# Kernel optimization log

Measured on AMD Instinct MI355X. Metric: run time of the kernel, lower is better.

Reference implementation:

```python
import jax, jax.numpy as jnp
import numpy as np

EPS = 1e-8
LN_EPS = 1e-6
B, S_IN, F, D, NH, MLP, L, O = 32, 512, 16, 512, 8, 2048, 4, 8
HD = D // NH

def softplus(x):
    return jnp.log1p(jnp.exp(x))

def apply_rope(x):
    # x: [B, S, D]; RoPE over full d_model, as in the original
    S, d = x.shape[1], x.shape[2]
    x1, x2 = x[..., ::2], x[..., 1::2]
    theta = jnp.arange(S)[:, None] / 10000 ** (jnp.arange(0, d, 2) / d)
    c, s = jnp.cos(theta)[None], jnp.sin(theta)[None]
    x1r = x1 * c - x2 * s
    x2r = x1 * s + x2 * c
    return jnp.stack([x1r, x2r], axis=-1).reshape(x.shape)

def layer_norm(x, g, b):
    mu = jnp.mean(x, axis=-1, keepdims=True)
    var = jnp.mean(jnp.square(x - mu), axis=-1, keepdims=True)
    return (x - mu) * jax.lax.rsqrt(var + LN_EPS) * g + b

def setup_inputs() -> dict:
    key = jax.random.key(0)
    ks = jax.random.split(key, 32)
    n = jax.random.normal
    d = {
        "x": n(ks[0], (B, S_IN, F), jnp.float32),
        "W_in": n(ks[1], (F, D)) * (1.0 / np.sqrt(F)),
        "b_in": jnp.zeros((D,)),
        "cls_tokens": n(ks[2], (1, O, D)) * 0.02,
        "Wqkv": n(ks[3], (L, D, 3 * D)) * (1.0 / np.sqrt(D)),
        "bqkv": jnp.zeros((L, 3 * D)),
        "Wo": n(ks[4], (L, D, D)) * (1.0 / np.sqrt(D)),
        "bo": jnp.zeros((L, D)),
        "ln1_g": jnp.ones((L, D)), "ln1_b": jnp.zeros((L, D)),
        "Wm1": n(ks[5], (L, D, MLP)) * (1.0 / np.sqrt(D)),
        "bm1": jnp.zeros((L, MLP)),
        "Wm2": n(ks[6], (L, MLP, D)) * (1.0 / np.sqrt(MLP)),
        "bm2": jnp.zeros((L, D)),
        "ln2_g": jnp.ones((L, D)), "ln2_b": jnp.zeros((L, D)),
        "Wh": n(ks[7], (O, D, D)) * (1.0 / np.sqrt(D)),
        "bh": jnp.zeros((O, D)),
        "mu_wmu": n(ks[8], (O, D)) * (1.0 / np.sqrt(D)),
        "mu_wrho": n(ks[9], (O, D)) * 0.001,
        "mu_bmu": jnp.zeros((O,)),
        "mu_brho": n(ks[10], (O,)) * 0.001,
        "lv_wmu": n(ks[11], (O, D)) * (1.0 / np.sqrt(D)),
        "lv_wrho": n(ks[12], (O, D)) * 0.001,
        "lv_bmu": jnp.zeros((O,)),
        "lv_brho": n(ks[13], (O,)) * 0.001,
        "eps_mu_w": n(ks[14], (O, D)),
        "eps_mu_b": n(ks[15], (O,)),
        "eps_lv_w": n(ks[16], (O, D)),
        "eps_lv_b": n(ks[17], (O,)),
    }
    return d

def reference(x, W_in, b_in, cls_tokens, Wqkv, bqkv, Wo, bo, ln1_g, ln1_b,
              Wm1, bm1, Wm2, bm2, ln2_g, ln2_b, Wh, bh,
              mu_wmu, mu_wrho, mu_bmu, mu_brho,
              lv_wmu, lv_wrho, lv_bmu, lv_brho,
              eps_mu_w, eps_mu_b, eps_lv_w, eps_lv_b):
    h = x @ W_in + b_in                                     # [B, S_IN, D]
    cls = jnp.tile(cls_tokens, (h.shape[0], 1, 1))
    h = jnp.concatenate([cls, h], axis=1)                   # [B, S, D]
    Bt, S, d = h.shape
    for l in range(L):
        qkv = h @ Wqkv[l] + bqkv[l]
        q, k, v = jnp.split(qkv, 3, axis=-1)
        q, k = apply_rope(q), apply_rope(k)
        q = q.reshape(Bt, S, NH, HD).transpose(0, 2, 1, 3)
        k = k.reshape(Bt, S, NH, HD).transpose(0, 2, 1, 3)
        v = v.reshape(Bt, S, NH, HD).transpose(0, 2, 1, 3)
        scores = jnp.einsum('bhid,bhjd->bhij', q, k) / jnp.sqrt(jnp.float32(HD))
        attn = jax.nn.softmax(scores, axis=-1)              # dropout off (eval)
        out = jnp.einsum('bhij,bhjd->bhid', attn, v)
        out = out.transpose(0, 2, 1, 3).reshape(Bt, S, d)
        out = out @ Wo[l] + bo[l]
        h = layer_norm(h + out, ln1_g[l], ln1_b[l])
        m = jax.nn.relu(h @ Wm1[l] + bm1[l]) @ Wm2[l] + bm2[l]
        h = layer_norm(h + m, ln2_g[l], ln2_b[l])
    x_cls = h[:, :O, :]                                     # [B, O, D]
    hid = jax.nn.relu(jnp.einsum('bod,odh->boh', x_cls, Wh) + bh[None])
    def var_head(wmu, wrho, bmu, brho, ew, eb):
        w = wmu + (softplus(wrho) + EPS) * ew               # [O, D]
        b = bmu + (softplus(brho) + EPS) * eb               # [O]
        return jnp.einsum('boh,oh->bo', hid, w) + b[None]
    mu = var_head(mu_wmu, mu_wrho, mu_bmu, mu_brho, eps_mu_w, eps_mu_b)
    lv = var_head(lv_wmu, lv_wrho, lv_bmu, lv_brho, eps_lv_w, eps_lv_b)
    lv = jnp.log(EPS + softplus(lv))
    return (mu, lv)
```

## Files before the change

kernel.cpp:

```cpp
#include <hip/hip_runtime.h>
#include <cstdint>


#define BATCH   32
#define SEQ     520
#define SP      576
#define DIM     512
#define NHEAD   8
#define HDIM    64
#define MLPD    2048
#define NLAYER  4
#define NROW    (BATCH * SEQ)
#define NPAIR   256

typedef __attribute__((ext_vector_type(4))) float  f32x4;
typedef __attribute__((ext_vector_type(8))) short  short8;

__device__ __forceinline__ unsigned short f2bf(float f) {
    unsigned u = __float_as_uint(f);
    unsigned r = (u + 0x7fffu + ((u >> 16) & 1u)) >> 16;
    return (unsigned short)r;
}
__device__ __forceinline__ float bf2f(short s) {
    return __uint_as_float(((unsigned)(unsigned short)s) << 16);
}
__device__ __forceinline__ float wred_sum(float v) {
    #pragma unroll
    for (int off = 32; off; off >>= 1) v += __shfl_xor(v, off);
    return v;
}

__device__ __forceinline__ void gload16(const void* g, void* l) {
    __builtin_amdgcn_global_load_lds(
        (const __attribute__((address_space(1))) unsigned int*)g,
        (__attribute__((address_space(3))) unsigned int*)l,
        16, 0, 0);
}

__global__ __launch_bounds__(256) void k_wconv(const float* __restrict__ src,
                                               short* __restrict__ dst,
                                               int K, int N) {
    src += (size_t)blockIdx.z * K * N;
    dst += (size_t)blockIdx.z * K * N;
    int n0 = blockIdx.x * 64, k0 = blockIdx.y * 64;
    __shared__ float t[64][65];
    int tid = threadIdx.x;
    int r = tid >> 2, cq = (tid & 3) * 16;
    const float* sp = src + (size_t)(k0 + r) * N + n0 + cq;
    #pragma unroll
    for (int e = 0; e < 16; e += 4) {
        float4 v = *(const float4*)(sp + e);
        t[r][cq + e] = v.x; t[r][cq + e + 1] = v.y;
        t[r][cq + e + 2] = v.z; t[r][cq + e + 3] = v.w;
    }
    __syncthreads();
    int n = tid >> 2, kq = (tid & 3) * 16;
    short* dp = dst + (size_t)(n0 + n) * K + k0 + kq;
    short8 o0, o1;
    #pragma unroll
    for (int e = 0; e < 8; e++) o0[e] = (short)f2bf(t[kq + e][n]);
    #pragma unroll
    for (int e = 0; e < 8; e++) o1[e] = (short)f2bf(t[kq + 8 + e][n]);
    *(short8*)dp = o0;
    *(short8*)(dp + 8) = o1;
}

__global__ void k_rope_tab(float2* __restrict__ tab) {
    int s = blockIdx.x, i = threadIdx.x;
    float fr = powf(10000.f, -2.f * (float)i / 512.f);
    float th = (float)s * fr;
    float sn, cn;
    sincosf(th, &sn, &cn);
    tab[s * NPAIR + i] = make_float2(cn, sn);
}

__global__ __launch_bounds__(256) void k_in_proj(const float* __restrict__ x,
                                                 const float* __restrict__ Wi,
                                                 const float* __restrict__ bi,
                                                 const float* __restrict__ cls,
                                                 short* __restrict__ hb) {
    int row = blockIdx.x;
    int b = row / SEQ, s = row % SEQ;
    bool is_cls = s < 8;
    float xr[16];
    if (!is_cls) {
        const float* xp = x + (size_t)(b * 512 + (s - 8)) * 16;
        #pragma unroll
        for (int f = 0; f < 16; f++) xr[f] = xp[f];
    }
    for (int c = threadIdx.x; c < DIM; c += 256) {
        float v;
        if (is_cls) {
            v = cls[s * DIM + c];
        } else {
            v = bi[c];
            #pragma unroll
            for (int f = 0; f < 16; f++) v = fmaf(xr[f], Wi[f * DIM + c], v);
        }
        hb[(size_t)row * DIM + c] = (short)f2bf(v);
    }
}

template <int BK, bool RELU>
__global__ __launch_bounds__(256) void k_gemm(const short* __restrict__ A,
                                              const short* __restrict__ Bt,
                                              const float* __restrict__ bias,
                                              short* __restrict__ Cout,
                                              int N, int K) {
    constexpr int NB  = BK / 8;
    constexpr int MSK = NB - 1;
    constexpr int RPG = 1024 / (BK * 2);
    constexpr int GPW = 32 / RPG;
    __shared__ __align__(16) short As[2][128 * BK];
    __shared__ __align__(16) short Bs[2][128 * BK];
    const int tid = threadIdx.x;
    const int w = tid >> 6, l = tid & 63;

    const int chunk = gridDim.x >> 3;
    const int t = (blockIdx.x & 7) * chunk + (blockIdx.x >> 3);
    const int C = N >> 7;
    const int brow = (t / C) * 128, bcol = (t % C) * 128;

    const int srow = l / NB;
    const int sblk = l & MSK;
    const int soff = ((sblk ^ (srow & MSK)) * 8);
    const int fr = l & 15, t4 = l >> 4;
    const int wr = (w >> 1) * 64, wc = (w & 1) * 64;

    const short* Ab = A  + (size_t)(brow + w * 32 + srow) * K + soff;
    const short* Bb = Bt + (size_t)(bcol + w * 32 + srow) * K + soff;

    f32x4 acc[4][4];
    #pragma unroll
    for (int m = 0; m < 4; m++)
        #pragma unroll
        for (int n = 0; n < 4; n++) acc[m][n] = (f32x4){0.f, 0.f, 0.f, 0.f};

    auto stage = [&](int ko, int pb) {
        #pragma unroll
        for (int i = 0; i < GPW; i++)
            gload16(Ab + (size_t)(i * RPG) * K + ko,
                    &As[pb][(w * 32 + i * RPG) * BK]);
        #pragma unroll
        for (int i = 0; i < GPW; i++)
            gload16(Bb + (size_t)(i * RPG) * K + ko,
                    &Bs[pb][(w * 32 + i * RPG) * BK]);
    };

    const int nk = K / BK;
    stage(0, 0);
    __syncthreads();

    for (int kt = 0; kt < nk; ++kt) {
        const int cur = kt & 1;
        if (kt + 1 < nk) stage((kt + 1) * BK, cur ^ 1);
        __builtin_amdgcn_sched_barrier(0);

        short8 af[4][BK / 32], bf[4][BK / 32];
        #pragma unroll
        for (int m = 0; m < 4; m++) {
            int r = wr + m * 16 + fr;
            #pragma unroll
            for (int kk = 0; kk < BK / 32; kk++)
                af[m][kk] = *(const short8*)
                    &As[cur][r * BK + (((kk * 4 + t4) ^ (r & MSK)) * 8)];
        }
        #pragma unroll
        for (int n = 0; n < 4; n++) {
            int r = wc + n * 16 + fr;
            #pragma unroll
            for (int kk = 0; kk < BK / 32; kk++)
                bf[n][kk] = *(const short8*)
                    &Bs[cur][r * BK + (((kk * 4 + t4) ^ (r & MSK)) * 8)];
        }
        #pragma unroll
        for (int kk = 0; kk < BK / 32; kk++)
            #pragma unroll
            for (int m = 0; m < 4; m++)
                #pragma unroll
                for (int n = 0; n < 4; n++)
                    acc[m][n] = __builtin_amdgcn_mfma_f32_16x16x32_bf16(
                        af[m][kk], bf[n][kk], acc[m][n], 0, 0, 0);
        __syncthreads();
    }

    const int r0 = (l >> 4) * 4, c0 = l & 15;
    #pragma unroll
    for (int m = 0; m < 4; m++) {
        #pragma unroll
        for (int n = 0; n < 4; n++) {
            int col = bcol + wc + n * 16 + c0;
            float bv = bias[col];
            #pragma unroll
            for (int q = 0; q < 4; q++) {
                int row = brow + wr + m * 16 + r0 + q;
                float v = acc[m][n][q] + bv;
                if (RELU) v = fmaxf(v, 0.f);
                Cout[(size_t)row * N + col] = (short)f2bf(v);
            }
        }
    }
}

__global__ __launch_bounds__(256) void k_kvprep(const short* __restrict__ qkv,
                                                const float2* __restrict__ tab,
                                                short* __restrict__ kbuf,
                                                short* __restrict__ vtbuf) {
    int bx = blockIdx.x;
    int jt = bx % 9, bh = bx / 9, b = bh >> 3, h = bh & 7;
    int tid = threadIdx.x;
    int row = tid >> 2, ch = tid & 3;
    int s = jt * 64 + row;
    bool valid = s < SEQ;
    size_t g = (size_t)(b * SEQ + (valid ? s : 0)) * 1536;

    short8 ok0 = (short8)0, ok1 = (short8)0;
    if (valid) {
        short8 k0 = *(const short8*)(qkv + g + 512 + h * 64 + ch * 16);
        short8 k1 = *(const short8*)(qkv + g + 512 + h * 64 + ch * 16 + 8);
        #pragma unroll
        for (int pp = 0; pp < 4; pp++) {
            float2 cs = tab[s * NPAIR + h * 32 + ch * 8 + pp];
            float x1 = bf2f(k0[2 * pp]), x2 = bf2f(k0[2 * pp + 1]);
            ok0[2 * pp]     = (short)f2bf(x1 * cs.x - x2 * cs.y);
            ok0[2 * pp + 1] = (short)f2bf(x1 * cs.y + x2 * cs.x);
            cs = tab[s * NPAIR + h * 32 + ch * 8 + 4 + pp];
            x1 = bf2f(k1[2 * pp]); x2 = bf2f(k1[2 * pp + 1]);
            ok1[2 * pp]     = (short)f2bf(x1 * cs.x - x2 * cs.y);
            ok1[2 * pp + 1] = (short)f2bf(x1 * cs.y + x2 * cs.x);
        }
    }
    short* kd = kbuf + ((size_t)bh * SP + jt * 64 + row) * 64 + ch * 16;
    *(short8*)kd = ok0;
    *(short8*)(kd + 8) = ok1;

    __shared__ short vt[64][72];
    short8 v0 = (short8)0, v1 = (short8)0;
    if (valid) {
        v0 = *(const short8*)(qkv + g + 1024 + h * 64 + ch * 16);
        v1 = *(const short8*)(qkv + g + 1024 + h * 64 + ch * 16 + 8);
    }
    *(short8*)&vt[row][ch * 16] = v0;
    *(short8*)&vt[row][ch * 16 + 8] = v1;
    __syncthreads();
    int d = row;
    short8 w0, w1;
    #pragma unroll
    for (int e = 0; e < 8; e++) w0[e] = vt[ch * 16 + e][d];
    #pragma unroll
    for (int e = 0; e < 8; e++) w1[e] = vt[ch * 16 + 8 + e][d];
    short* vd = vtbuf + ((size_t)bh * 64 + d) * SP + jt * 64 + ch * 16;
    *(short8*)vd = w0;
    *(short8*)(vd + 8) = w1;
}

__global__ __launch_bounds__(256) void k_attn_mfma(const short* __restrict__ qkv,
                                                   const short* __restrict__ kbuf,
                                                   const short* __restrict__ vtbuf,
                                                   const float2* __restrict__ tab,
                                                   short* __restrict__ aob) {
    __shared__ __align__(16) short Kl[2][64 * 64];
    __shared__ __align__(16) short Vl[2][64 * 64];
    __shared__ __align__(16) short sP[4][16][72];
    const int tid = threadIdx.x;
    const int w = tid >> 6, l = tid & 63;
    const int c = l & 15, t4 = l >> 4;
    int bx = blockIdx.x;
    int qt = bx >> 8, bh = bx & 255, b = bh >> 3, h = bh & 7;

    int q0 = qt * 64 + w * 16;
    int qrow = q0 + c;
    int qr = qrow < SEQ ? qrow : SEQ - 1;
    size_t gq = (size_t)(b * SEQ + qr) * 1536 + h * 64;
    short8 qf0 = *(const short8*)(qkv + gq + t4 * 8);
    short8 qf1 = *(const short8*)(qkv + gq + 32 + t4 * 8);
    {
        const float2* tq = tab + (size_t)qr * NPAIR + h * 32;
        #pragma unroll
        for (int pp = 0; pp < 4; pp++) {
            float2 cs = tq[t4 * 4 + pp];
            float x1 = bf2f(qf0[2 * pp]), x2 = bf2f(qf0[2 * pp + 1]);
            qf0[2 * pp]     = (short)f2bf((x1 * cs.x - x2 * cs.y) * 0.125f);
            qf0[2 * pp + 1] = (short)f2bf((x1 * cs.y + x2 * cs.x) * 0.125f);
            cs = tq[16 + t4 * 4 + pp];
            x1 = bf2f(qf1[2 * pp]); x2 = bf2f(qf1[2 * pp + 1]);
            qf1[2 * pp]     = (short)f2bf((x1 * cs.x - x2 * cs.y) * 0.125f);
            qf1[2 * pp + 1] = (short)f2bf((x1 * cs.y + x2 * cs.x) * 0.125f);
        }
    }

    f32x4 o0 = {0,0,0,0}, o1 = {0,0,0,0}, o2 = {0,0,0,0}, o3 = {0,0,0,0};
    float mrow[4] = {-1e30f, -1e30f, -1e30f, -1e30f};
    float lrow[4] = {0.f, 0.f, 0.f, 0.f};

    const short* kb = kbuf + (size_t)bh * SP * 64;
    const short* vb = vtbuf + (size_t)bh * 64 * SP;
    const int r1 = w * 16 + (l >> 3);
    const int r2 = r1 + 8;
    const int blk = l & 7;

    auto stage = [&](int jt, int pb) {
        gload16(kb + ((size_t)(jt * 64 + r1)) * 64 + ((blk ^ (r1 & 7)) * 8),
                &Kl[pb][(w * 16) * 64]);
        gload16(kb + ((size_t)(jt * 64 + r2)) * 64 + ((blk ^ (r2 & 7)) * 8),
                &Kl[pb][(w * 16 + 8) * 64]);
        gload16(vb + (size_t)r1 * SP + jt * 64 + ((blk ^ (r1 & 7)) * 8),
                &Vl[pb][(w * 16) * 64]);
        gload16(vb + (size_t)r2 * SP + jt * 64 + ((blk ^ (r2 & 7)) * 8),
                &Vl[pb][(w * 16 + 8) * 64]);
    };

    stage(0, 0);
    __syncthreads();

    for (int jt = 0; jt < 9; jt++) {
        const int cur = jt & 1;
        if (jt + 1 < 9) stage(jt + 1, cur ^ 1);
        __builtin_amdgcn_sched_barrier(0);

        f32x4 s0 = {0,0,0,0}, s1 = {0,0,0,0}, s2 = {0,0,0,0}, s3 = {0,0,0,0};
        {
            int kr0 = c, kr1 = 16 + c, kr2 = 32 + c, kr3 = 48 + c;
            short8 kf;
            kf = *(const short8*)&Kl[cur][kr0 * 64 + ((t4 ^ (kr0 & 7)) * 8)];
            s0 = __builtin_amdgcn_mfma_f32_16x16x32_bf16(qf0, kf, s0, 0, 0, 0);
            kf = *(const short8*)&Kl[cur][kr0 * 64 + (((4 + t4) ^ (kr0 & 7)) * 8)];
            s0 = __builtin_amdgcn_mfma_f32_16x16x32_bf16(qf1, kf, s0, 0, 0, 0);
            kf = *(const short8*)&Kl[cur][kr1 * 64 + ((t4 ^ (kr1 & 7)) * 8)];
            s1 = __builtin_amdgcn_mfma_f32_16x16x32_bf16(qf0, kf, s1, 0, 0, 0);
            kf = *(const short8*)&Kl[cur][kr1 * 64 + (((4 + t4) ^ (kr1 & 7)) * 8)];
            s1 = __builtin_amdgcn_mfma_f32_16x16x32_bf16(qf1, kf, s1, 0, 0, 0);
            kf = *(const short8*)&Kl[cur][kr2 * 64 + ((t4 ^ (kr2 & 7)) * 8)];
            s2 = __builtin_amdgcn_mfma_f32_16x16x32_bf16(qf0, kf, s2, 0, 0, 0);
            kf = *(const short8*)&Kl[cur][kr2 * 64 + (((4 + t4) ^ (kr2 & 7)) * 8)];
            s2 = __builtin_amdgcn_mfma_f32_16x16x32_bf16(qf1, kf, s2, 0, 0, 0);
            kf = *(const short8*)&Kl[cur][kr3 * 64 + ((t4 ^ (kr3 & 7)) * 8)];
            s3 = __builtin_amdgcn_mfma_f32_16x16x32_bf16(qf0, kf, s3, 0, 0, 0);
            kf = *(const short8*)&Kl[cur][kr3 * 64 + (((4 + t4) ^ (kr3 & 7)) * 8)];
            s3 = __builtin_amdgcn_mfma_f32_16x16x32_bf16(qf1, kf, s3, 0, 0, 0);
        }

        if (jt == 8) {
            #pragma unroll
            for (int r = 0; r < 4; r++) {
                if (c >= 8) s0[r] = -1e30f;
                s1[r] = -1e30f; s2[r] = -1e30f; s3[r] = -1e30f;
            }
        }

        #pragma unroll
        for (int r = 0; r < 4; r++) {
            float mx = fmaxf(fmaxf(s0[r], s1[r]), fmaxf(s2[r], s3[r]));
            mx = fmaxf(mx, __shfl_xor(mx, 1));
            mx = fmaxf(mx, __shfl_xor(mx, 2));
            mx = fmaxf(mx, __shfl_xor(mx, 4));
            mx = fmaxf(mx, __shfl_xor(mx, 8));
            if (mx > mrow[r]) {
                float sc = __expf(mrow[r] - mx);
                mrow[r] = mx;
                lrow[r] *= sc;
                o0[r] *= sc; o1[r] *= sc; o2[r] *= sc; o3[r] *= sc;
            }
            float p0 = __expf(s0[r] - mrow[r]), p1 = __expf(s1[r] - mrow[r]);
            float p2 = __expf(s2[r] - mrow[r]), p3 = __expf(s3[r] - mrow[r]);
            float rs = p0 + p1 + p2 + p3;
            rs += __shfl_xor(rs, 1);
            rs += __shfl_xor(rs, 2);
            rs += __shfl_xor(rs, 4);
            rs += __shfl_xor(rs, 8);
            lrow[r] += rs;
            int q = t4 * 4 + r;
            sP[w][q][c]      = (short)f2bf(p0);
            sP[w][q][16 + c] = (short)f2bf(p1);
            sP[w][q][32 + c] = (short)f2bf(p2);
            sP[w][q][48 + c] = (short)f2bf(p3);
        }

        {
            short8 pf0 = *(const short8*)&sP[w][c][t4 * 8];
            short8 pf1 = *(const short8*)&sP[w][c][32 + t4 * 8];
            int vr0 = c, vr1 = 16 + c, vr2 = 32 + c, vr3 = 48 + c;
            short8 vf;
            vf = *(const short8*)&Vl[cur][vr0 * 64 + ((t4 ^ (vr0 & 7)) * 8)];
            o0 = __builtin_amdgcn_mfma_f32_16x16x32_bf16(pf0, vf, o0, 0, 0, 0);
            vf = *(const short8*)&Vl[cur][vr0 * 64 + (((4 + t4) ^ (vr0 & 7)) * 8)];
            o0 = __builtin_amdgcn_mfma_f32_16x16x32_bf16(pf1, vf, o0, 0, 0, 0);
            vf = *(const short8*)&Vl[cur][vr1 * 64 + ((t4 ^ (vr1 & 7)) * 8)];
            o1 = __builtin_amdgcn_mfma_f32_16x16x32_bf16(pf0, vf, o1, 0, 0, 0);
            vf = *(const short8*)&Vl[cur][vr1 * 64 + (((4 + t4) ^ (vr1 & 7)) * 8)];
            o1 = __builtin_amdgcn_mfma_f32_16x16x32_bf16(pf1, vf, o1, 0, 0, 0);
            vf = *(const short8*)&Vl[cur][vr2 * 64 + ((t4 ^ (vr2 & 7)) * 8)];
            o2 = __builtin_amdgcn_mfma_f32_16x16x32_bf16(pf0, vf, o2, 0, 0, 0);
            vf = *(const short8*)&Vl[cur][vr2 * 64 + (((4 + t4) ^ (vr2 & 7)) * 8)];
            o2 = __builtin_amdgcn_mfma_f32_16x16x32_bf16(pf1, vf, o2, 0, 0, 0);
            vf = *(const short8*)&Vl[cur][vr3 * 64 + ((t4 ^ (vr3 & 7)) * 8)];
            o3 = __builtin_amdgcn_mfma_f32_16x16x32_bf16(pf0, vf, o3, 0, 0, 0);
            vf = *(const short8*)&Vl[cur][vr3 * 64 + (((4 + t4) ^ (vr3 & 7)) * 8)];
            o3 = __builtin_amdgcn_mfma_f32_16x16x32_bf16(pf1, vf, o3, 0, 0, 0);
        }
        __syncthreads();
    }

    #pragma unroll
    for (int r = 0; r < 4; r++) {
        int q = q0 + t4 * 4 + r;
        if (q < SEQ) {
            float inv = 1.f / lrow[r];
            short* ao = aob + ((size_t)(b * SEQ + q)) * DIM + h * 64 + c;
            ao[0]  = (short)f2bf(o0[r] * inv);
            ao[16] = (short)f2bf(o1[r] * inv);
            ao[32] = (short)f2bf(o2[r] * inv);
            ao[48] = (short)f2bf(o3[r] * inv);
        }
    }
}

__global__ __launch_bounds__(256) void k_ln(short* __restrict__ hb,
                                            const short* __restrict__ delta,
                                            const float* __restrict__ g,
                                            const float* __restrict__ bta) {
    int row = blockIdx.x * 4 + (threadIdx.x >> 6);
    int l = threadIdx.x & 63;
    size_t base = (size_t)row * DIM + l * 8;
    short8 hv = *(const short8*)&hb[base];
    short8 dv = *(const short8*)&delta[base];
    float a[8];
    float s1 = 0.f, s2 = 0.f;
    #pragma unroll
    for (int e = 0; e < 8; e++) {
        a[e] = bf2f(hv[e]) + bf2f(dv[e]);
        s1 += a[e];
        s2 += a[e] * a[e];
    }
    s1 = wred_sum(s1);
    s2 = wred_sum(s2);
    float mu = s1 * (1.f / 512.f);
    float rr = rsqrtf(s2 * (1.f / 512.f) - mu * mu + 1e-6f);
    float4 g0 = *(const float4*)&g[l * 8];
    float4 g1 = *(const float4*)&g[l * 8 + 4];
    float4 b0 = *(const float4*)&bta[l * 8];
    float4 b1 = *(const float4*)&bta[l * 8 + 4];
    short8 o;
    o[0] = (short)f2bf((a[0] - mu) * rr * g0.x + b0.x);
    o[1] = (short)f2bf((a[1] - mu) * rr * g0.y + b0.y);
    o[2] = (short)f2bf((a[2] - mu) * rr * g0.z + b0.z);
    o[3] = (short)f2bf((a[3] - mu) * rr * g0.w + b0.w);
    o[4] = (short)f2bf((a[4] - mu) * rr * g1.x + b1.x);
    o[5] = (short)f2bf((a[5] - mu) * rr * g1.y + b1.y);
    o[6] = (short)f2bf((a[6] - mu) * rr * g1.z + b1.z);
    o[7] = (short)f2bf((a[7] - mu) * rr * g1.w + b1.w);
    *(short8*)&hb[base] = o;
}

__global__ __launch_bounds__(256) void k_hid(const short* __restrict__ hb,
                                             const float* __restrict__ Wh,
                                             const float* __restrict__ bh,
                                             float* __restrict__ hid) {
    int j = blockIdx.x * 256 + threadIdx.x;
    int o = blockIdx.y, b = blockIdx.z;
    const short* xr = hb + ((size_t)(b * SEQ + o)) * DIM;
    const float* wcol = Wh + (size_t)o * DIM * DIM + j;
    float acc = bh[o * DIM + j];
    #pragma unroll 8
    for (int d = 0; d < DIM; d++)
        acc = fmaf(bf2f(xr[d]), wcol[(size_t)d * DIM], acc);
    hid[((size_t)b * 8 + o) * DIM + j] = fmaxf(acc, 0.f);
}

__device__ __forceinline__ float softplus_f(float x) { return log1pf(expf(x)); }

__global__ __launch_bounds__(64) void k_var(const float* __restrict__ hid,
                                            const float* __restrict__ mu_wmu,
                                            const float* __restrict__ mu_wrho,
                                            const float* __restrict__ mu_bmu,
                                            const float* __restrict__ mu_brho,
                                            const float* __restrict__ lv_wmu,
                                            const float* __restrict__ lv_wrho,
                                            const float* __restrict__ lv_bmu,
                                            const float* __restrict__ lv_brho,
                                            const float* __restrict__ eps_mu_w,
                                            const float* __restrict__ eps_mu_b,
                                            const float* __restrict__ eps_lv_w,
                                            const float* __restrict__ eps_lv_b,
                                            float* __restrict__ out) {
    const float EPS = 1e-8f;
    int bo = blockIdx.x;
    int o = bo & 7;
    int l = threadIdx.x;
    float am = 0.f, al = 0.f;
    #pragma unroll
    for (int k = 0; k < 8; k++) {
        int d = k * 64 + l;
        int od = o * DIM + d;
        float hv = hid[(size_t)bo * DIM + d];
        am = fmaf(hv, mu_wmu[od] + (softplus_f(mu_wrho[od]) + EPS) * eps_mu_w[od], am);
        al = fmaf(hv, lv_wmu[od] + (softplus_f(lv_wrho[od]) + EPS) * eps_lv_w[od], al);
    }
    am = wred_sum(am);
    al = wred_sum(al);
    if (l == 0) {
        float mu = am + mu_bmu[o] + (softplus_f(mu_brho[o]) + EPS) * eps_mu_b[o];
        out[bo] = mu;
        float lvv = al + lv_bmu[o] + (softplus_f(lv_brho[o]) + EPS) * eps_lv_b[o];
        out[256 + bo] = logf(EPS + softplus_f(lvv));
    }
}

extern "C" void kernel_launch(void* const* d_in, const int* in_sizes, int n_in,
                              void* d_out, int out_size, void* d_ws, size_t ws_size,
                              hipStream_t stream) {
    const float* x      = (const float*)d_in[0];
    const float* W_in   = (const float*)d_in[1];
    const float* b_in   = (const float*)d_in[2];
    const float* cls    = (const float*)d_in[3];
    const float* Wqkv   = (const float*)d_in[4];
    const float* bqkv   = (const float*)d_in[5];
    const float* Wo     = (const float*)d_in[6];
    const float* bo     = (const float*)d_in[7];
    const float* ln1_g  = (const float*)d_in[8];
    const float* ln1_b  = (const float*)d_in[9];
    const float* Wm1    = (const float*)d_in[10];
    const float* bm1    = (const float*)d_in[11];
    const float* Wm2    = (const float*)d_in[12];
    const float* bm2    = (const float*)d_in[13];
    const float* ln2_g  = (const float*)d_in[14];
    const float* ln2_b  = (const float*)d_in[15];
    const float* Wh     = (const float*)d_in[16];
    const float* bh     = (const float*)d_in[17];
    const float* mu_wmu = (const float*)d_in[18];
    const float* mu_wrho= (const float*)d_in[19];
    const float* mu_bmu = (const float*)d_in[20];
    const float* mu_brho= (const float*)d_in[21];
    const float* lv_wmu = (const float*)d_in[22];
    const float* lv_wrho= (const float*)d_in[23];
    const float* lv_bmu = (const float*)d_in[24];
    const float* lv_brho= (const float*)d_in[25];
    const float* e_mu_w = (const float*)d_in[26];
    const float* e_mu_b = (const float*)d_in[27];
    const float* e_lv_w = (const float*)d_in[28];
    const float* e_lv_b = (const float*)d_in[29];
    float* out = (float*)d_out;

    char* p = (char*)d_ws;
    auto alloc = [&](size_t bytes) {
        char* r = p;
        p += (bytes + 255) & ~(size_t)255;
        return r;
    };
    const size_t qkv_bytes = (size_t)NROW * 1536 * 2;
    const size_t kbuf_bytes = (size_t)BATCH * NHEAD * SP * 64 * 2;
    const size_t attn_bytes = qkv_bytes + 2 * kbuf_bytes + 512;
    const size_t mid_bytes = (size_t)NROW * MLPD * 2;
    char*   U1    =          alloc(attn_bytes > mid_bytes ? attn_bytes : mid_bytes);
    short*  qkv   = (short*)U1;
    short*  kbuf  = (short*)(U1 + ((qkv_bytes + 255) & ~(size_t)255));
    short*  vtbuf = kbuf + kbuf_bytes / 2;
    short*  mid   = (short*)U1;
    short*  hb    = (short*) alloc((size_t)NROW * DIM * 2);
    short*  deltab= (short*) alloc((size_t)NROW * DIM * 2);
    short*  aob   = (short*) alloc((size_t)NROW * DIM * 2);
    short*  wqkvt = (short*) alloc((size_t)NLAYER * 1536 * 512 * 2);
    short*  wot   = (short*) alloc((size_t)NLAYER * 512 * 512 * 2);
    short*  wm1t  = (short*) alloc((size_t)NLAYER * 2048 * 512 * 2);
    short*  wm2t  = (short*) alloc((size_t)NLAYER * 512 * 2048 * 2);
    float2* ropet = (float2*)alloc((size_t)SEQ * NPAIR * 8);
    float*  hid   = (float*) alloc((size_t)256 * DIM * 4);

    k_wconv<<<dim3(24, 8, 4), 256, 0, stream>>>(Wqkv, wqkvt, 512, 1536);
    k_wconv<<<dim3(8, 8, 4),  256, 0, stream>>>(Wo,   wot,   512, 512);
    k_wconv<<<dim3(32, 8, 4), 256, 0, stream>>>(Wm1,  wm1t,  512, 2048);
    k_wconv<<<dim3(8, 32, 4), 256, 0, stream>>>(Wm2,  wm2t,  2048, 512);
    k_rope_tab<<<SEQ, NPAIR, 0, stream>>>(ropet);
    k_in_proj<<<NROW, 256, 0, stream>>>(x, W_in, b_in, cls, hb);

    const int RT = NROW / 128;
    for (int l = 0; l < NLAYER; l++) {
        k_gemm<32, false><<<RT * 12, 256, 0, stream>>>(
            hb, wqkvt + (size_t)l * 1536 * 512, bqkv + l * 1536, qkv, 1536, 512);
        k_kvprep<<<BATCH * NHEAD * 9, 256, 0, stream>>>(qkv, ropet, kbuf, vtbuf);
        k_attn_mfma<<<9 * 256, 256, 0, stream>>>(qkv, kbuf, vtbuf, ropet, aob);
        k_gemm<64, false><<<RT * 4, 256, 0, stream>>>(
            aob, wot + (size_t)l * 512 * 512, bo + l * 512, deltab, 512, 512);
        k_ln<<<NROW / 4, 256, 0, stream>>>(hb, deltab, ln1_g + l * 512, ln1_b + l * 512);
        k_gemm<32, true><<<RT * 16, 256, 0, stream>>>(
            hb, wm1t + (size_t)l * 2048 * 512, bm1 + l * 2048, mid, 2048, 512);
        k_gemm<64, false><<<RT * 4, 256, 0, stream>>>(
            mid, wm2t + (size_t)l * 512 * 2048, bm2 + l * 512, deltab, 512, 2048);
        k_ln<<<NROW / 4, 256, 0, stream>>>(hb, deltab, ln2_g + l * 512, ln2_b + l * 512);
    }

    k_hid<<<dim3(2, 8, 32), 256, 0, stream>>>(hb, Wh, bh, hid);
    k_var<<<256, 64, 0, stream>>>(hid, mu_wmu, mu_wrho, mu_bmu, mu_brho,
                                  lv_wmu, lv_wrho, lv_bmu, lv_brho,
                                  e_mu_w, e_mu_b, e_lv_w, e_lv_b, out);
}
```

Measured before the change: 1.232 ms.

## Fuse residual add into GEMM epilogue, use packed bf16 cvt and exp2 softmax

Moves the residual add from the layernorm kernels into the output-projection and MLP2 GEMM epilogues, so layernorm reads only one input tensor. Replaces software bf16 rounding with the hardware v_cvt_pk_bf16_f32 instruction across several kernels. Attention folds log2(e) into the Q scale, uses the hardware exp2, skips the row-max rescale when no lane exceeds the running max by more than a threshold, defers the row-sum shuffle reduction to the end, and raises wave priority around the MFMA blocks. The GEMM epilogue now does an extra strided read of the residual, and the lazy rescale lets exponents grow up to 2^8 before renormalising.

```diff
diff --git a/kernel.cpp b/kernel.cpp
--- a/kernel.cpp
+++ b/kernel.cpp
@@ -24,6 +24,16 @@
 __device__ __forceinline__ float bf2f(short s) {
     return __uint_as_float(((unsigned)(unsigned short)s) << 16);
 }
+__device__ __forceinline__ unsigned cvt_pk_bf16(float lo, float hi) {
+    unsigned r;
+    asm("v_cvt_pk_bf16_f32 %0, %1, %2" : "=v"(r) : "v"(lo), "v"(hi));
+    return r;
+}
+__device__ __forceinline__ float exp2_hw(float x) {
+    float r;
+    asm("v_exp_f32 %0, %1" : "=v"(r) : "v"(x));
+    return r;
+}
 __device__ __forceinline__ float wred_sum(float v) {
     #pragma unroll
     for (int off = 32; off; off >>= 1) v += __shfl_xor(v, off);
@@ -56,13 +66,15 @@
     __syncthreads();
     int n = tid >> 2, kq = (tid & 3) * 16;
     short* dp = dst + (size_t)(n0 + n) * K + k0 + kq;
-    short8 o0, o1;
-    #pragma unroll
-    for (int e = 0; e < 8; e++) o0[e] = (short)f2bf(t[kq + e][n]);
-    #pragma unroll
-    for (int e = 0; e < 8; e++) o1[e] = (short)f2bf(t[kq + 8 + e][n]);
-    *(short8*)dp = o0;
-    *(short8*)(dp + 8) = o1;
+    unsigned o0[4], o1[4];
+    #pragma unroll
+    for (int e = 0; e < 4; e++)
+        o0[e] = cvt_pk_bf16(t[kq + 2 * e][n], t[kq + 2 * e + 1][n]);
+    #pragma unroll
+    for (int e = 0; e < 4; e++)
+        o1[e] = cvt_pk_bf16(t[kq + 8 + 2 * e][n], t[kq + 9 + 2 * e][n]);
+    *(uint4*)dp = make_uint4(o0[0], o0[1], o0[2], o0[3]);
+    *(uint4*)(dp + 8) = make_uint4(o1[0], o1[1], o1[2], o1[3]);
 }
 
 __global__ void k_rope_tab(float2* __restrict__ tab) {
@@ -101,10 +113,11 @@
     }
 }
 
-template <int BK, bool RELU>
+template <int BK, bool RELU, bool ADDRES>
 __global__ __launch_bounds__(256) void k_gemm(const short* __restrict__ A,
                                               const short* __restrict__ Bt,
                                               const float* __restrict__ bias,
+                                              const short* __restrict__ Res,
                                               short* __restrict__ Cout,
                                               int N, int K) {
     constexpr int NB  = BK / 8;
@@ -195,6 +208,7 @@
             for (int q = 0; q < 4; q++) {
                 int row = brow + wr + m * 16 + r0 + q;
                 float v = acc[m][n][q] + bv;
+                if (ADDRES) v += bf2f(Res[(size_t)row * N + col]);
                 if (RELU) v = fmaxf(v, 0.f);
                 Cout[(size_t)row * N + col] = (short)f2bf(v);
             }
@@ -218,16 +232,16 @@
     if (valid) {
         short8 k0 = *(const short8*)(qkv + g + 512 + h * 64 + ch * 16);
         short8 k1 = *(const short8*)(qkv + g + 512 + h * 64 + ch * 16 + 8);
+        unsigned* u0 = (unsigned*)&ok0;
+        unsigned* u1 = (unsigned*)&ok1;
         #pragma unroll
         for (int pp = 0; pp < 4; pp++) {
             float2 cs = tab[s * NPAIR + h * 32 + ch * 8 + pp];
             float x1 = bf2f(k0[2 * pp]), x2 = bf2f(k0[2 * pp + 1]);
-            ok0[2 * pp]     = (short)f2bf(x1 * cs.x - x2 * cs.y);
-            ok0[2 * pp + 1] = (short)f2bf(x1 * cs.y + x2 * cs.x);
+            u0[pp] = cvt_pk_bf16(x1 * cs.x - x2 * cs.y, x1 * cs.y + x2 * cs.x);
             cs = tab[s * NPAIR + h * 32 + ch * 8 + 4 + pp];
             x1 = bf2f(k1[2 * pp]); x2 = bf2f(k1[2 * pp + 1]);
-            ok1[2 * pp]     = (short)f2bf(x1 * cs.x - x2 * cs.y);
-            ok1[2 * pp + 1] = (short)f2bf(x1 * cs.y + x2 * cs.x);
+            u1[pp] = cvt_pk_bf16(x1 * cs.x - x2 * cs.y, x1 * cs.y + x2 * cs.x);
         }
     }
     short* kd = kbuf + ((size_t)bh * SP + jt * 64 + row) * 64 + ch * 16;
@@ -268,6 +282,7 @@
     int bx = blockIdx.x;
     int qt = bx >> 8, bh = bx & 255, b = bh >> 3, h = bh & 7;
 
+    const float QSC = 0.125f * 1.44269504f;
     int q0 = qt * 64 + w * 16;
     int qrow = q0 + c;
     int qr = qrow < SEQ ? qrow : SEQ - 1;
@@ -276,16 +291,18 @@
     short8 qf1 = *(const short8*)(qkv + gq + 32 + t4 * 8);
     {
         const float2* tq = tab + (size_t)qr * NPAIR + h * 32;
+        unsigned* u0 = (unsigned*)&qf0;
+        unsigned* u1 = (unsigned*)&qf1;
         #pragma unroll
         for (int pp = 0; pp < 4; pp++) {
             float2 cs = tq[t4 * 4 + pp];
             float x1 = bf2f(qf0[2 * pp]), x2 = bf2f(qf0[2 * pp + 1]);
-            qf0[2 * pp]     = (short)f2bf((x1 * cs.x - x2 * cs.y) * 0.125f);
-            qf0[2 * pp + 1] = (short)f2bf((x1 * cs.y + x2 * cs.x) * 0.125f);
+            u0[pp] = cvt_pk_bf16((x1 * cs.x - x2 * cs.y) * QSC,
+                                 (x1 * cs.y + x2 * cs.x) * QSC);
             cs = tq[16 + t4 * 4 + pp];
             x1 = bf2f(qf1[2 * pp]); x2 = bf2f(qf1[2 * pp + 1]);
-            qf1[2 * pp]     = (short)f2bf((x1 * cs.x - x2 * cs.y) * 0.125f);
-            qf1[2 * pp + 1] = (short)f2bf((x1 * cs.y + x2 * cs.x) * 0.125f);
+            u1[pp] = cvt_pk_bf16((x1 * cs.x - x2 * cs.y) * QSC,
+                                 (x1 * cs.y + x2 * cs.x) * QSC);
         }
     }
 
@@ -319,6 +336,7 @@
         __builtin_amdgcn_sched_barrier(0);
 
         f32x4 s0 = {0,0,0,0}, s1 = {0,0,0,0}, s2 = {0,0,0,0}, s3 = {0,0,0,0};
+        __builtin_amdgcn_s_setprio(1);
         {
             int kr0 = c, kr1 = 16 + c, kr2 = 32 + c, kr3 = 48 + c;
             short8 kf;
@@ -339,6 +357,7 @@
             kf = *(const short8*)&Kl[cur][kr3 * 64 + (((4 + t4) ^ (kr3 & 7)) * 8)];
             s3 = __builtin_amdgcn_mfma_f32_16x16x32_bf16(qf1, kf, s3, 0, 0, 0);
         }
+        __builtin_amdgcn_s_setprio(0);
 
         if (jt == 8) {
             #pragma unroll
@@ -350,32 +369,35 @@
 
         #pragma unroll
         for (int r = 0; r < 4; r++) {
-            float mx = fmaxf(fmaxf(s0[r], s1[r]), fmaxf(s2[r], s3[r]));
-            mx = fmaxf(mx, __shfl_xor(mx, 1));
-            mx = fmaxf(mx, __shfl_xor(mx, 2));
-            mx = fmaxf(mx, __shfl_xor(mx, 4));
-            mx = fmaxf(mx, __shfl_xor(mx, 8));
-            if (mx > mrow[r]) {
-                float sc = __expf(mrow[r] - mx);
-                mrow[r] = mx;
-                lrow[r] *= sc;
-                o0[r] *= sc; o1[r] *= sc; o2[r] *= sc; o3[r] *= sc;
+            float pmax = fmaxf(fmaxf(s0[r], s1[r]), fmaxf(s2[r], s3[r]));
+            if (!__all(pmax <= mrow[r] + 8.f)) {
+                float mx = pmax;
+                mx = fmaxf(mx, __shfl_xor(mx, 1));
+                mx = fmaxf(mx, __shfl_xor(mx, 2));
+                mx = fmaxf(mx, __shfl_xor(mx, 4));
+                mx = fmaxf(mx, __shfl_xor(mx, 8));
+                if (mx > mrow[r]) {
+                    float sc = exp2_hw(mrow[r] - mx);
+                    mrow[r] = mx;
+                    lrow[r] *= sc;
+                    o0[r] *= sc; o1[r] *= sc; o2[r] *= sc; o3[r] *= sc;
+                }
             }
-            float p0 = __expf(s0[r] - mrow[r]), p1 = __expf(s1[r] - mrow[r]);
-            float p2 = __expf(s2[r] - mrow[r]), p3 = __expf(s3[r] - mrow[r]);
-            float rs = p0 + p1 + p2 + p3;
-            rs += __shfl_xor(rs, 1);
-            rs += __shfl_xor(rs, 2);
-            rs += __shfl_xor(rs, 4);
-            rs += __shfl_xor(rs, 8);
-            lrow[r] += rs;
+            float p0 = exp2_hw(s0[r] - mrow[r]);
+            float p1 = exp2_hw(s1[r] - mrow[r]);
+            float p2 = exp2_hw(s2[r] - mrow[r]);
+            float p3 = exp2_hw(s3[r] - mrow[r]);
+            lrow[r] += (p0 + p1) + (p2 + p3);
+            unsigned pk01 = cvt_pk_bf16(p0, p1);
+            unsigned pk23 = cvt_pk_bf16(p2, p3);
             int q = t4 * 4 + r;
-            sP[w][q][c]      = (short)f2bf(p0);
-            sP[w][q][16 + c] = (short)f2bf(p1);
-            sP[w][q][32 + c] = (short)f2bf(p2);
-            sP[w][q][48 + c] = (short)f2bf(p3);
-        }
-
+            sP[w][q][c]      = (short)(pk01 & 0xffff);
+            sP[w][q][16 + c] = (short)(pk01 >> 16);
+            sP[w][q][32 + c] = (short)(pk23 & 0xffff);
+            sP[w][q][48 + c] = (short)(pk23 >> 16);
+        }
+
+        __builtin_amdgcn_s_setprio(1);
         {
             short8 pf0 = *(const short8*)&sP[w][c][t4 * 8];
             short8 pf1 = *(const short8*)&sP[w][c][32 + t4 * 8];
@@ -398,14 +420,20 @@
             vf = *(const short8*)&Vl[cur][vr3 * 64 + (((4 + t4) ^ (vr3 & 7)) * 8)];
             o3 = __builtin_amdgcn_mfma_f32_16x16x32_bf16(pf1, vf, o3, 0, 0, 0);
         }
+        __builtin_amdgcn_s_setprio(0);
         __syncthreads();
     }
 
     #pragma unroll
     for (int r = 0; r < 4; r++) {
+        float s = lrow[r];
+        s += __shfl_xor(s, 1);
+        s += __shfl_xor(s, 2);
+        s += __shfl_xor(s, 4);
+        s += __shfl_xor(s, 8);
         int q = q0 + t4 * 4 + r;
         if (q < SEQ) {
-            float inv = 1.f / lrow[r];
+            float inv = 1.f / s;
             short* ao = aob + ((size_t)(b * SEQ + q)) * DIM + h * 64 + c;
             ao[0]  = (short)f2bf(o0[r] * inv);
             ao[16] = (short)f2bf(o1[r] * inv);
@@ -416,19 +444,18 @@
 }
 
 __global__ __launch_bounds__(256) void k_ln(short* __restrict__ hb,
-                                            const short* __restrict__ delta,
+                                            const short* __restrict__ sum,
                                             const float* __restrict__ g,
                                             const float* __restrict__ bta) {
     int row = blockIdx.x * 4 + (threadIdx.x >> 6);
     int l = threadIdx.x & 63;
     size_t base = (size_t)row * DIM + l * 8;
-    short8 hv = *(const short8*)&hb[base];
-    short8 dv = *(const short8*)&delta[base];
+    short8 hv = *(const short8*)&sum[base];
     float a[8];
     float s1 = 0.f, s2 = 0.f;
     #pragma unroll
     for (int e = 0; e < 8; e++) {
-        a[e] = bf2f(hv[e]) + bf2f(dv[e]);
+        a[e] = bf2f(hv[e]);
         s1 += a[e];
         s2 += a[e] * a[e];
     }
@@ -440,16 +467,16 @@
     float4 g1 = *(const float4*)&g[l * 8 + 4];
     float4 b0 = *(const float4*)&bta[l * 8];
     float4 b1 = *(const float4*)&bta[l * 8 + 4];
-    short8 o;
-    o[0] = (short)f2bf((a[0] - mu) * rr * g0.x + b0.x);
-    o[1] = (short)f2bf((a[1] - mu) * rr * g0.y + b0.y);
-    o[2] = (short)f2bf((a[2] - mu) * rr * g0.z + b0.z);
-    o[3] = (short)f2bf((a[3] - mu) * rr * g0.w + b0.w);
-    o[4] = (short)f2bf((a[4] - mu) * rr * g1.x + b1.x);
-    o[5] = (short)f2bf((a[5] - mu) * rr * g1.y + b1.y);
-    o[6] = (short)f2bf((a[6] - mu) * rr * g1.z + b1.z);
-    o[7] = (short)f2bf((a[7] - mu) * rr * g1.w + b1.w);
-    *(short8*)&hb[base] = o;
+    unsigned o[4];
+    o[0] = cvt_pk_bf16((a[0] - mu) * rr * g0.x + b0.x,
+                       (a[1] - mu) * rr * g0.y + b0.y);
+    o[1] = cvt_pk_bf16((a[2] - mu) * rr * g0.z + b0.z,
+                       (a[3] - mu) * rr * g0.w + b0.w);
+    o[2] = cvt_pk_bf16((a[4] - mu) * rr * g1.x + b1.x,
+                       (a[5] - mu) * rr * g1.y + b1.y);
+    o[3] = cvt_pk_bf16((a[6] - mu) * rr * g1.z + b1.z,
+                       (a[7] - mu) * rr * g1.w + b1.w);
+    *(uint4*)&hb[base] = make_uint4(o[0], o[1], o[2], o[3]);
 }
 
 __global__ __launch_bounds__(256) void k_hid(const short* __restrict__ hb,
@@ -575,17 +602,17 @@
 
     const int RT = NROW / 128;
     for (int l = 0; l < NLAYER; l++) {
-        k_gemm<32, false><<<RT * 12, 256, 0, stream>>>(
-            hb, wqkvt + (size_t)l * 1536 * 512, bqkv + l * 1536, qkv, 1536, 512);
+        k_gemm<32, false, false><<<RT * 12, 256, 0, stream>>>(
+            hb, wqkvt + (size_t)l * 1536 * 512, bqkv + l * 1536, nullptr, qkv, 1536, 512);
         k_kvprep<<<BATCH * NHEAD * 9, 256, 0, stream>>>(qkv, ropet, kbuf, vtbuf);
         k_attn_mfma<<<9 * 256, 256, 0, stream>>>(qkv, kbuf, vtbuf, ropet, aob);
-        k_gemm<64, false><<<RT * 4, 256, 0, stream>>>(
-            aob, wot + (size_t)l * 512 * 512, bo + l * 512, deltab, 512, 512);
+        k_gemm<64, false, true><<<RT * 4, 256, 0, stream>>>(
+            aob, wot + (size_t)l * 512 * 512, bo + l * 512, hb, deltab, 512, 512);
         k_ln<<<NROW / 4, 256, 0, stream>>>(hb, deltab, ln1_g + l * 512, ln1_b + l * 512);
-        k_gemm<32, true><<<RT * 16, 256, 0, stream>>>(
-            hb, wm1t + (size_t)l * 2048 * 512, bm1 + l * 2048, mid, 2048, 512);
-        k_gemm<64, false><<<RT * 4, 256, 0, stream>>>(
-            mid, wm2t + (size_t)l * 512 * 2048, bm2 + l * 512, deltab, 512, 2048);
+        k_gemm<32, true, false><<<RT * 16, 256, 0, stream>>>(
+            hb, wm1t + (size_t)l * 2048 * 512, bm1 + l * 2048, nullptr, mid, 2048, 512);
+        k_gemm<64, false, true><<<RT * 4, 256, 0, stream>>>(
+            mid, wm2t + (size_t)l * 512 * 2048, bm2 + l * 512, hb, deltab, 512, 2048);
         k_ln<<<NROW / 4, 256, 0, stream>>>(hb, deltab, ln2_g + l * 512, ln2_b + l * 512);
     }
 
```

Result: faster. 1.157 ms (-6.0%).
